# Kernel tuning notes

Measured on AMD Instinct MI355X. Metric: run time of the kernel, lower is better.

Reference implementation:

```python
import jax, jax.numpy as jnp
import numpy as np
from jax import lax

R = 0.7          # ball-query radius
K = 32           # max neighbors per ball
STRIDE = 32      # spatial stride -> M = N // STRIDE anchors
COUT = 1024      # mlp_planes[0]


def fps(pts, M):
    """Furthest point sampling. pts: [N,3] -> int32 [M] indices (starts at 0, like CUDA FPS)."""
    N = pts.shape[0]

    def step(carry, _):
        d2, last = carry
        dist = jnp.sum((pts - pts[last]) ** 2, axis=-1)
        d2 = jnp.minimum(d2, dist)
        return (d2, jnp.argmax(d2).astype(jnp.int32)), last

    init = (jnp.full((N,), 1e10, dtype=pts.dtype), jnp.int32(0))
    _, idxs = lax.scan(step, init, None, length=M)
    return idxs


def ball_query(neigh, anchor):
    """neigh: [N,3], anchor: [M,3] -> int32 [M,K]: first K in-radius neighbor indices,
    padded with the first valid index (matching pointnet2 ball_query semantics)."""
    N = neigh.shape[0]
    d2 = jnp.sum((anchor[:, None, :] - neigh[None, :, :]) ** 2, axis=-1)  # [M,N]
    key = jnp.where(d2 < R * R, jnp.arange(N), N)  # valid points keep their position
    order = jnp.argsort(key, axis=-1)[:, :K]       # stable: first-in-order valid indices
    valid = jnp.take_along_axis(key, order, axis=-1) < N
    return jnp.where(valid, order, order[:, :1])


def setup_inputs() -> dict:
    key = jax.random.key(0)
    k1, k2 = jax.random.split(key)
    xyzs = jax.random.uniform(k1, (4, 16, 2048, 3), dtype=jnp.float32)  # points in unit cube
    w_d = jax.random.normal(k2, (COUT, 4), dtype=jnp.float32) * 0.1     # conv_d 1x1 weight
    return {"xyzs": xyzs, "w_d": w_d}


def reference(xyzs, w_d):
    B, T, N, _ = xyzs.shape
    M = N // STRIDE
    # replicate temporal padding [1,1]
    pad = jnp.concatenate([xyzs[:, :1], xyzs, xyzs[:, -1:]], axis=1)  # [B,T+2,N,3]

    anchors_src = pad[:, 1:-1].reshape(B * T, N, 3)
    aidx = jax.vmap(lambda p: fps(p, M))(anchors_src)                         # [BT,M]
    anchor = jnp.take_along_axis(anchors_src, aidx[..., None], axis=1)        # [BT,M,3]

    feat = None
    for dt in (-1, 0, 1):  # temporal kernel taps
        neigh = pad[:, 1 + dt: 1 + dt + T].reshape(B * T, N, 3)
        idx = jax.vmap(ball_query)(neigh, anchor)                             # [BT,M,K]
        grouped = jnp.take_along_axis(
            neigh, idx.reshape(B * T, M * K)[..., None], axis=1
        ).reshape(B * T, M, K, 3)
        disp = grouped - anchor[:, :, None, :]                                # xyz displacement
        d4 = jnp.concatenate(
            [disp, jnp.full((B * T, M, K, 1), float(dt), disp.dtype)], axis=-1
        )                                                                     # [BT,M,K,4]
        f = jax.nn.relu(jnp.einsum('nmkc,oc->nmko', d4, w_d))                 # 1x1 conv + ReLU
        f = jnp.max(f, axis=2)                                                # spatial max pool -> [BT,M,C]
        feat = f if feat is None else feat + f                                # temporal sum pool

    new_xyzs = anchor.reshape(B, T, M, 3)
    new_features = feat.reshape(B, T, M, COUT).transpose(0, 1, 3, 2)          # [B,T,C,M]
    return new_xyzs, new_features
```

## Files before the change

kernel.cpp:

```cpp
#include <hip/hip_runtime.h>
#include <hip/hip_fp16.h>

#define NB 4
#define NT 16
#define NN 2048
#define NM 64
#define NK 32
#define NC 1024

static __device__ inline __half2 h2max(__half2 a, __half2 b) {
    unsigned int ai = *(unsigned int*)&a, bi = *(unsigned int*)&b, di;
    asm("v_pk_max_f16 %0, %1, %2" : "=v"(di) : "v"(ai), "v"(bi));
    return *(__half2*)&di;
}
static __device__ inline unsigned long long u64max(unsigned long long a, unsigned long long b) {
    return a > b ? a : b;
}

#define DPP_MAX_STEP(v, ctrl)                                                   \
    do {                                                                        \
        const int _mv = __builtin_amdgcn_update_dpp(                            \
            __float_as_int(v), __float_as_int(v), (ctrl), 0xf, 0xf, false);     \
        (v) = fmaxf((v), __int_as_float(_mv));                                  \
    } while (0)

__global__ __launch_bounds__(256) void fps_kernel(const float* __restrict__ xyzs,
                                                  float* __restrict__ out_xyz) {
    const int bt = blockIdx.x;
    const float* pts = xyzs + (size_t)bt * NN * 3;
    __shared__ __align__(16) float sP[NN * 3];
    __shared__ unsigned long long sPart[2][4];
    __shared__ float sAnchor[NM * 3];
    const int tid = threadIdx.x;
    const int lane = tid & 63, wave = tid >> 6;
    float wpt[24];
    {
        const float4* pv = (const float4*)pts + (size_t)tid * 6;
        #pragma unroll
        for (int i = 0; i < 6; ++i) {
            const float4 f = pv[i];
            ((float4*)sP)[tid * 6 + i] = f;
            wpt[4 * i + 0] = f.x; wpt[4 * i + 1] = f.y; wpt[4 * i + 2] = f.z; wpt[4 * i + 3] = f.w;
        }
    }
    float px[8], py[8], pz[8], d2[8];
    #pragma unroll
    for (int j = 0; j < 8; ++j) {
        px[j] = wpt[3 * j + 0]; py[j] = wpt[3 * j + 1]; pz[j] = wpt[3 * j + 2];
        d2[j] = 1e10f;
    }
    __syncthreads();
    int last = 0;
    for (int it = 0; it < NM; ++it) {
        const float lx = sP[last * 3 + 0], ly = sP[last * 3 + 1], lz = sP[last * 3 + 2];
        if (tid == 0) {
            sAnchor[it * 3 + 0] = lx; sAnchor[it * 3 + 1] = ly; sAnchor[it * 3 + 2] = lz;
        }
        float bv = -1.0f; int bp = 0;
        #pragma unroll
        for (int j = 0; j < 8; ++j) {
            const float dx = __fsub_rn(px[j], lx), dy = __fsub_rn(py[j], ly), dz = __fsub_rn(pz[j], lz);
            const float d = __fadd_rn(__fadd_rn(__fmul_rn(dx, dx), __fmul_rn(dy, dy)), __fmul_rn(dz, dz));
            d2[j] = fminf(d2[j], d);
            if (d2[j] > bv) { bv = d2[j]; bp = tid * 8 + j; }
        }
        float v = bv;
        DPP_MAX_STEP(v, 0x111);
        DPP_MAX_STEP(v, 0x112);
        DPP_MAX_STEP(v, 0x114);
        DPP_MAX_STEP(v, 0x118);
        DPP_MAX_STEP(v, 0x142);
        DPP_MAX_STEP(v, 0x143);
        const float vmax = __int_as_float(__builtin_amdgcn_readlane(__float_as_int(v), 63));
        const unsigned long long tied = __ballot(bv == vmax);
        const int srcLane = (int)(__ffsll((long long)tied) - 1);
        const int idxw = __shfl(bp, srcLane, 64);
        if (lane == 0)
            sPart[it & 1][wave] = ((unsigned long long)__float_as_uint(vmax) << 32)
                                | (unsigned)(NN - 1 - idxw);
        __syncthreads();
        const unsigned long long key =
            u64max(u64max(sPart[it & 1][0], sPart[it & 1][1]),
                   u64max(sPart[it & 1][2], sPart[it & 1][3]));
        last = NN - 1 - (int)(key & 0xffffffffull);
    }
    __syncthreads();
    for (int i = tid; i < NM * 3; i += 256)
        out_xyz[bt * NM * 3 + i] = sAnchor[i];
}

__global__ __launch_bounds__(256) void bq_kernel(const float* __restrict__ xyzs,
                                                 const float* __restrict__ anchors,
                                                 unsigned int* __restrict__ disp) {
    const int tid = threadIdx.x;
    const int lane = tid & 63, w = tid >> 6;
    const int q = blockIdx.x * 4 + w;
    const int bt = q / (NM * 3);
    const int r = q - bt * (NM * 3);
    const int m = r / 3, tap = r - m * 3;
    const int b = bt >> 4, t = bt & 15;
    __shared__ float sD[4][3][NK];
    const float ax = anchors[(bt * NM + m) * 3 + 0];
    const float ay = anchors[(bt * NM + m) * 3 + 1];
    const float az = anchors[(bt * NM + m) * 3 + 2];
    int tsrc = t + tap - 1;
    tsrc = tsrc < 0 ? 0 : (tsrc > NT - 1 ? NT - 1 : tsrc);
    const float* npts = xyzs + ((size_t)(b * NT + tsrc)) * NN * 3;
    int cnt = 0;
    for (int rr = 0; rr < NN / 64 && cnt < NK; ++rr) {
        const int n = rr * 64 + lane;
        const float dx = __fsub_rn(npts[n * 3 + 0], ax);
        const float dy = __fsub_rn(npts[n * 3 + 1], ay);
        const float dz = __fsub_rn(npts[n * 3 + 2], az);
        const float d2v = __fadd_rn(__fadd_rn(__fmul_rn(dx, dx), __fmul_rn(dy, dy)), __fmul_rn(dz, dz));
        const bool valid = d2v < 0.49f;
        const unsigned long long mask = __ballot(valid);
        const int pos = cnt + (int)__popcll(mask & ((1ull << lane) - 1ull));
        if (valid && pos < NK) {
            sD[w][0][pos] = dx; sD[w][1][pos] = dy; sD[w][2][pos] = dz;
        }
        cnt += (int)__popcll(mask);
    }
    if (cnt < NK) {
        float fx, fy, fz;
        if (cnt > 0) {
            fx = sD[w][0][0]; fy = sD[w][1][0]; fz = sD[w][2][0];
        } else {
            fx = __fsub_rn(npts[0], ax); fy = __fsub_rn(npts[1], ay); fz = __fsub_rn(npts[2], az);
        }
        if (lane >= cnt && lane < NK) {
            sD[w][0][lane] = fx; sD[w][1][lane] = fy; sD[w][2][lane] = fz;
        }
    }
    if (lane < 48) {
        const int c = lane >> 4, j = lane & 15;
        const __half2 hv = __float22half2_rn(make_float2(sD[w][c][2 * j], sD[w][c][2 * j + 1]));
        disp[(size_t)q * 48 + lane] = *(const unsigned int*)&hv;
    }
}

__global__ __launch_bounds__(256) void conv_kernel(const unsigned int* __restrict__ disp,
                                                   const float* __restrict__ wd,
                                                   float* __restrict__ feat) {
    const int blk = blockIdx.x;
    const int bt = blk >> 4;
    const int inner = blk & 15;
    const int mh = inner >> 2, cq = inner & 3;
    const int tid = threadIdx.x;
    const int lane = tid & 63, w = tid >> 6;
    const int m0 = mh * 16 + w * 4;
    const int c0 = cq * 256 + lane;
    float4 wv[4]; __half2 wx[4], wy[4], wz[4];
    #pragma unroll
    for (int r = 0; r < 4; ++r) {
        wv[r] = ((const float4*)wd)[c0 + 64 * r];
        wx[r] = __float2half2_rn(wv[r].x);
        wy[r] = __float2half2_rn(wv[r].y);
        wz[r] = __float2half2_rn(wv[r].z);
    }
    float acc[4][4];
    #pragma unroll
    for (int r = 0; r < 4; ++r)
        #pragma unroll
        for (int mi = 0; mi < 4; ++mi) acc[r][mi] = 0.0f;

    #pragma unroll
    for (int mi = 0; mi < 4; ++mi) {
        #pragma unroll
        for (int tap = 0; tap < 3; ++tap) {
            const uint4* dp = (const uint4*)(disp + ((size_t)((bt * NM + m0 + mi) * 3 + tap)) * 48);
            uint4 u[12];
            #pragma unroll
            for (int i = 0; i < 12; ++i) u[i] = dp[i];
            const unsigned int* uw = (const unsigned int*)u;
            __half2 a[4];
            #pragma unroll
            for (int j = 0; j < 16; ++j) {
                const __half2 hx = *(const __half2*)&uw[j];
                const __half2 hy = *(const __half2*)&uw[16 + j];
                const __half2 hz = *(const __half2*)&uw[32 + j];
                #pragma unroll
                for (int r = 0; r < 4; ++r) {
                    const __half2 s = __hfma2(wx[r], hx, __hfma2(wy[r], hy, __hmul2(wz[r], hz)));
                    a[r] = (j == 0) ? s : h2max(a[r], s);
                }
            }
            const float dtf = (float)(tap - 1);
            #pragma unroll
            for (int r = 0; r < 4; ++r) {
                const float mx = fmaxf(__low2float(a[r]), __high2float(a[r]));
                acc[r][mi] += fmaxf(0.0f, mx + wv[r].w * dtf);
            }
        }
    }
    #pragma unroll
    for (int r = 0; r < 4; ++r) {
        float* dst = feat + ((size_t)bt * NC + c0 + 64 * r) * NM + m0;
        *(float4*)dst = make_float4(acc[r][0], acc[r][1], acc[r][2], acc[r][3]);
    }
}

extern "C" void kernel_launch(void* const* d_in, const int* in_sizes, int n_in,
                              void* d_out, int out_size, void* d_ws, size_t ws_size,
                              hipStream_t stream) {
    const float* xyzs = (const float*)d_in[0];
    const float* wd   = (const float*)d_in[1];
    float* out_xyz = (float*)d_out;
    float* featp   = out_xyz + NB * NT * NM * 3;
    unsigned int* dispw = (unsigned int*)d_ws;
    hipLaunchKernelGGL(fps_kernel, dim3(NB * NT), dim3(256), 0, stream, xyzs, out_xyz);
    hipLaunchKernelGGL(bq_kernel, dim3(NB * NT * NM * 3 / 4), dim3(256), 0, stream,
                       xyzs, out_xyz, dispw);
    hipLaunchKernelGGL(conv_kernel, dim3(1024), dim3(256), 0, stream,
                       dispw, wd, featp);
}
```

Measured before the change: 123.6 us.

## Carry FPS winner coordinates through reduction and halve conv per-block work

```diff
diff --git a/kernel.cpp b/kernel.cpp
--- a/kernel.cpp
+++ b/kernel.cpp
@@ -13,9 +13,6 @@
     asm("v_pk_max_f16 %0, %1, %2" : "=v"(di) : "v"(ai), "v"(bi));
     return *(__half2*)&di;
 }
-static __device__ inline unsigned long long u64max(unsigned long long a, unsigned long long b) {
-    return a > b ? a : b;
-}
 
 #define DPP_MAX_STEP(v, ctrl)                                                   \
     do {                                                                        \
@@ -24,13 +21,18 @@
         (v) = fmaxf((v), __int_as_float(_mv));                                  \
     } while (0)
 
+static __device__ inline float readlane_f(float x, int l) {
+    return __int_as_float(__builtin_amdgcn_readlane(__float_as_int(x), l));
+}
+
 __global__ __launch_bounds__(256) void fps_kernel(const float* __restrict__ xyzs,
                                                   float* __restrict__ out_xyz) {
     const int bt = blockIdx.x;
     const float* pts = xyzs + (size_t)bt * NN * 3;
-    __shared__ __align__(16) float sP[NN * 3];
-    __shared__ unsigned long long sPart[2][4];
+    __shared__ unsigned long long sKey[2][4];
+    __shared__ __align__(16) float sCand[2][4][4];
     __shared__ float sAnchor[NM * 3];
+    __shared__ float sInit[3];
     const int tid = threadIdx.x;
     const int lane = tid & 63, wave = tid >> 6;
     float wpt[24];
@@ -39,30 +41,29 @@
         #pragma unroll
         for (int i = 0; i < 6; ++i) {
             const float4 f = pv[i];
-            ((float4*)sP)[tid * 6 + i] = f;
             wpt[4 * i + 0] = f.x; wpt[4 * i + 1] = f.y; wpt[4 * i + 2] = f.z; wpt[4 * i + 3] = f.w;
         }
     }
-    float px[8], py[8], pz[8], d2[8];
+    float px[8], py[8], pz[8], d2v[8];
     #pragma unroll
     for (int j = 0; j < 8; ++j) {
         px[j] = wpt[3 * j + 0]; py[j] = wpt[3 * j + 1]; pz[j] = wpt[3 * j + 2];
-        d2[j] = 1e10f;
-    }
+        d2v[j] = 1e10f;
+    }
+    if (tid == 0) { sInit[0] = px[0]; sInit[1] = py[0]; sInit[2] = pz[0]; }
     __syncthreads();
-    int last = 0;
+    float ax = sInit[0], ay = sInit[1], az = sInit[2];
     for (int it = 0; it < NM; ++it) {
-        const float lx = sP[last * 3 + 0], ly = sP[last * 3 + 1], lz = sP[last * 3 + 2];
         if (tid == 0) {
-            sAnchor[it * 3 + 0] = lx; sAnchor[it * 3 + 1] = ly; sAnchor[it * 3 + 2] = lz;
-        }
-        float bv = -1.0f; int bp = 0;
+            sAnchor[it * 3 + 0] = ax; sAnchor[it * 3 + 1] = ay; sAnchor[it * 3 + 2] = az;
+        }
+        float bv = -1.0f; int bj = 0;
         #pragma unroll
         for (int j = 0; j < 8; ++j) {
-            const float dx = __fsub_rn(px[j], lx), dy = __fsub_rn(py[j], ly), dz = __fsub_rn(pz[j], lz);
+            const float dx = __fsub_rn(px[j], ax), dy = __fsub_rn(py[j], ay), dz = __fsub_rn(pz[j], az);
             const float d = __fadd_rn(__fadd_rn(__fmul_rn(dx, dx), __fmul_rn(dy, dy)), __fmul_rn(dz, dz));
-            d2[j] = fminf(d2[j], d);
-            if (d2[j] > bv) { bv = d2[j]; bp = tid * 8 + j; }
+            d2v[j] = fminf(d2v[j], d);
+            if (d2v[j] > bv) { bv = d2v[j]; bj = j; }
         }
         float v = bv;
         DPP_MAX_STEP(v, 0x111);
@@ -71,18 +72,42 @@
         DPP_MAX_STEP(v, 0x118);
         DPP_MAX_STEP(v, 0x142);
         DPP_MAX_STEP(v, 0x143);
-        const float vmax = __int_as_float(__builtin_amdgcn_readlane(__float_as_int(v), 63));
+        const float vmax = readlane_f(v, 63);
         const unsigned long long tied = __ballot(bv == vmax);
-        const int srcLane = (int)(__ffsll((long long)tied) - 1);
-        const int idxw = __shfl(bp, srcLane, 64);
-        if (lane == 0)
-            sPart[it & 1][wave] = ((unsigned long long)__float_as_uint(vmax) << 32)
-                                | (unsigned)(NN - 1 - idxw);
+        const int src = (int)(__ffsll((long long)tied) - 1);
+        const float cx0 = (bj & 1) ? px[1] : px[0], cx1 = (bj & 1) ? px[3] : px[2];
+        const float cx2 = (bj & 1) ? px[5] : px[4], cx3 = (bj & 1) ? px[7] : px[6];
+        const float cy0 = (bj & 1) ? py[1] : py[0], cy1 = (bj & 1) ? py[3] : py[2];
+        const float cy2 = (bj & 1) ? py[5] : py[4], cy3 = (bj & 1) ? py[7] : py[6];
+        const float cz0 = (bj & 1) ? pz[1] : pz[0], cz1 = (bj & 1) ? pz[3] : pz[2];
+        const float cz2 = (bj & 1) ? pz[5] : pz[4], cz3 = (bj & 1) ? pz[7] : pz[6];
+        const float cxa = (bj & 2) ? cx1 : cx0, cxb = (bj & 2) ? cx3 : cx2;
+        const float cya = (bj & 2) ? cy1 : cy0, cyb = (bj & 2) ? cy3 : cy2;
+        const float cza = (bj & 2) ? cz1 : cz0, czb = (bj & 2) ? cz3 : cz2;
+        const float cx = (bj & 4) ? cxb : cxa;
+        const float cy = (bj & 4) ? cyb : cya;
+        const float cz = (bj & 4) ? czb : cza;
+        const int idx = tid * 8 + bj;
+        const int widx = __builtin_amdgcn_readlane(idx, src);
+        const float wx = readlane_f(cx, src);
+        const float wy = readlane_f(cy, src);
+        const float wz = readlane_f(cz, src);
+        const int par = it & 1;
+        if (lane == 0) {
+            sKey[par][wave] = ((unsigned long long)__float_as_uint(vmax) << 32)
+                            | (unsigned)(NN - 1 - widx);
+            *(float4*)&sCand[par][wave][0] = make_float4(wx, wy, wz, 0.0f);
+        }
         __syncthreads();
-        const unsigned long long key =
-            u64max(u64max(sPart[it & 1][0], sPart[it & 1][1]),
-                   u64max(sPart[it & 1][2], sPart[it & 1][3]));
-        last = NN - 1 - (int)(key & 0xffffffffull);
+        unsigned long long bk = sKey[par][0];
+        float4 bc = *(const float4*)&sCand[par][0][0];
+        #pragma unroll
+        for (int i = 1; i < 4; ++i) {
+            const unsigned long long ki = sKey[par][i];
+            const float4 ci = *(const float4*)&sCand[par][i][0];
+            if (ki > bk) { bk = ki; bc = ci; }
+        }
+        ax = bc.x; ay = bc.y; az = bc.z;
     }
     __syncthreads();
     for (int i = tid; i < NM * 3; i += 256)
@@ -139,64 +164,68 @@
     }
 }
 
-__global__ __launch_bounds__(256) void conv_kernel(const unsigned int* __restrict__ disp,
-                                                   const float* __restrict__ wd,
-                                                   float* __restrict__ feat) {
+__global__ __launch_bounds__(256, 8) void conv_kernel(const unsigned int* __restrict__ disp,
+                                                      const float* __restrict__ wd,
+                                                      float* __restrict__ feat) {
     const int blk = blockIdx.x;
-    const int bt = blk >> 4;
-    const int inner = blk & 15;
+    const int bt = blk >> 5;
+    const int inner = blk & 31;
     const int mh = inner >> 2, cq = inner & 3;
     const int tid = threadIdx.x;
     const int lane = tid & 63, w = tid >> 6;
-    const int m0 = mh * 16 + w * 4;
+    const int m0 = mh * 8 + w * 2;
     const int c0 = cq * 256 + lane;
-    float4 wv[4]; __half2 wx[4], wy[4], wz[4];
+    __half2 wx[4], wy[4], wz[4]; float ww[4];
     #pragma unroll
     for (int r = 0; r < 4; ++r) {
-        wv[r] = ((const float4*)wd)[c0 + 64 * r];
-        wx[r] = __float2half2_rn(wv[r].x);
-        wy[r] = __float2half2_rn(wv[r].y);
-        wz[r] = __float2half2_rn(wv[r].z);
-    }
-    float acc[4][4];
-    #pragma unroll
-    for (int r = 0; r < 4; ++r)
-        #pragma unroll
-        for (int mi = 0; mi < 4; ++mi) acc[r][mi] = 0.0f;
-
-    #pragma unroll
-    for (int mi = 0; mi < 4; ++mi) {
+        const float4 wv = ((const float4*)wd)[c0 + 64 * r];
+        wx[r] = __float2half2_rn(wv.x);
+        wy[r] = __float2half2_rn(wv.y);
+        wz[r] = __float2half2_rn(wv.z);
+        ww[r] = wv.w;
+    }
+    float acc[4][2];
+    #pragma unroll
+    for (int r = 0; r < 4; ++r) { acc[r][0] = 0.0f; acc[r][1] = 0.0f; }
+
+    #pragma unroll
+    for (int mi = 0; mi < 2; ++mi) {
         #pragma unroll
         for (int tap = 0; tap < 3; ++tap) {
             const uint4* dp = (const uint4*)(disp + ((size_t)((bt * NM + m0 + mi) * 3 + tap)) * 48);
-            uint4 u[12];
-            #pragma unroll
-            for (int i = 0; i < 12; ++i) u[i] = dp[i];
-            const unsigned int* uw = (const unsigned int*)u;
             __half2 a[4];
             #pragma unroll
-            for (int j = 0; j < 16; ++j) {
-                const __half2 hx = *(const __half2*)&uw[j];
-                const __half2 hy = *(const __half2*)&uw[16 + j];
-                const __half2 hz = *(const __half2*)&uw[32 + j];
+            for (int h = 0; h < 2; ++h) {
+                const uint4 ux0 = dp[2 * h],     ux1 = dp[2 * h + 1];
+                const uint4 uy0 = dp[4 + 2 * h], uy1 = dp[5 + 2 * h];
+                const uint4 uz0 = dp[8 + 2 * h], uz1 = dp[9 + 2 * h];
+                const unsigned int X[8] = {ux0.x, ux0.y, ux0.z, ux0.w, ux1.x, ux1.y, ux1.z, ux1.w};
+                const unsigned int Y[8] = {uy0.x, uy0.y, uy0.z, uy0.w, uy1.x, uy1.y, uy1.z, uy1.w};
+                const unsigned int Z[8] = {uz0.x, uz0.y, uz0.z, uz0.w, uz1.x, uz1.y, uz1.z, uz1.w};
                 #pragma unroll
-                for (int r = 0; r < 4; ++r) {
-                    const __half2 s = __hfma2(wx[r], hx, __hfma2(wy[r], hy, __hmul2(wz[r], hz)));
-                    a[r] = (j == 0) ? s : h2max(a[r], s);
+                for (int j = 0; j < 8; ++j) {
+                    const __half2 hx = *(const __half2*)&X[j];
+                    const __half2 hy = *(const __half2*)&Y[j];
+                    const __half2 hz = *(const __half2*)&Z[j];
+                    #pragma unroll
+                    for (int r = 0; r < 4; ++r) {
+                        const __half2 s = __hfma2(wx[r], hx, __hfma2(wy[r], hy, __hmul2(wz[r], hz)));
+                        a[r] = (h == 0 && j == 0) ? s : h2max(a[r], s);
+                    }
                 }
             }
             const float dtf = (float)(tap - 1);
             #pragma unroll
             for (int r = 0; r < 4; ++r) {
                 const float mx = fmaxf(__low2float(a[r]), __high2float(a[r]));
-                acc[r][mi] += fmaxf(0.0f, mx + wv[r].w * dtf);
+                acc[r][mi] += fmaxf(0.0f, mx + ww[r] * dtf);
             }
         }
     }
     #pragma unroll
     for (int r = 0; r < 4; ++r) {
         float* dst = feat + ((size_t)bt * NC + c0 + 64 * r) * NM + m0;
-        *(float4*)dst = make_float4(acc[r][0], acc[r][1], acc[r][2], acc[r][3]);
+        *(float2*)dst = make_float2(acc[r][0], acc[r][1]);
     }
 }
 
@@ -211,6 +240,6 @@
     hipLaunchKernelGGL(fps_kernel, dim3(NB * NT), dim3(256), 0, stream, xyzs, out_xyz);
     hipLaunchKernelGGL(bq_kernel, dim3(NB * NT * NM * 3 / 4), dim3(256), 0, stream,
                        xyzs, out_xyz, dispw);
-    hipLaunchKernelGGL(conv_kernel, dim3(1024), dim3(256), 0, stream,
+    hipLaunchKernelGGL(conv_kernel, dim3(2048), dim3(256), 0, stream,
                        dispw, wd, featp);
 }
```

New measurement: 132.6 us. 7.3% more time.

## Run FPS in a single wavefront to drop per-iteration block barriers

Applied to the files above, without the earlier changes.

```diff
diff --git a/kernel.cpp b/kernel.cpp
--- a/kernel.cpp
+++ b/kernel.cpp
@@ -13,9 +13,6 @@
     asm("v_pk_max_f16 %0, %1, %2" : "=v"(di) : "v"(ai), "v"(bi));
     return *(__half2*)&di;
 }
-static __device__ inline unsigned long long u64max(unsigned long long a, unsigned long long b) {
-    return a > b ? a : b;
-}
 
 #define DPP_MAX_STEP(v, ctrl)                                                   \
     do {                                                                        \
@@ -24,46 +21,62 @@
         (v) = fmaxf((v), __int_as_float(_mv));                                  \
     } while (0)
 
-__global__ __launch_bounds__(256) void fps_kernel(const float* __restrict__ xyzs,
-                                                  float* __restrict__ out_xyz) {
+static __device__ inline float readlane_f(float x, int l) {
+    return __int_as_float(__builtin_amdgcn_readlane(__float_as_int(x), l));
+}
+
+__global__ __launch_bounds__(64, 1) void fps_kernel(const float* __restrict__ xyzs,
+                                                    float* __restrict__ out_xyz) {
     const int bt = blockIdx.x;
     const float* pts = xyzs + (size_t)bt * NN * 3;
     __shared__ __align__(16) float sP[NN * 3];
-    __shared__ unsigned long long sPart[2][4];
-    __shared__ float sAnchor[NM * 3];
-    const int tid = threadIdx.x;
-    const int lane = tid & 63, wave = tid >> 6;
-    float wpt[24];
+    const int lane = threadIdx.x;
+    float arr[96];
     {
-        const float4* pv = (const float4*)pts + (size_t)tid * 6;
-        #pragma unroll
-        for (int i = 0; i < 6; ++i) {
+        const float4* pv = (const float4*)pts + (size_t)lane * 24;
+        #pragma unroll
+        for (int i = 0; i < 24; ++i) {
             const float4 f = pv[i];
-            ((float4*)sP)[tid * 6 + i] = f;
-            wpt[4 * i + 0] = f.x; wpt[4 * i + 1] = f.y; wpt[4 * i + 2] = f.z; wpt[4 * i + 3] = f.w;
-        }
-    }
-    float px[8], py[8], pz[8], d2[8];
-    #pragma unroll
-    for (int j = 0; j < 8; ++j) {
-        px[j] = wpt[3 * j + 0]; py[j] = wpt[3 * j + 1]; pz[j] = wpt[3 * j + 2];
-        d2[j] = 1e10f;
-    }
-    __syncthreads();
-    int last = 0;
+            ((float4*)sP)[lane * 24 + i] = f;
+            arr[4 * i + 0] = f.x; arr[4 * i + 1] = f.y; arr[4 * i + 2] = f.z; arr[4 * i + 3] = f.w;
+        }
+    }
+    float px[32], py[32], pz[32], d2[32];
+    #pragma unroll
+    for (int p = 0; p < 32; ++p) {
+        px[p] = arr[3 * p + 0]; py[p] = arr[3 * p + 1]; pz[p] = arr[3 * p + 2];
+        d2[p] = 1e10f;
+    }
+    float ax = readlane_f(px[0], 0), ay = readlane_f(py[0], 0), az = readlane_f(pz[0], 0);
     for (int it = 0; it < NM; ++it) {
-        const float lx = sP[last * 3 + 0], ly = sP[last * 3 + 1], lz = sP[last * 3 + 2];
-        if (tid == 0) {
-            sAnchor[it * 3 + 0] = lx; sAnchor[it * 3 + 1] = ly; sAnchor[it * 3 + 2] = lz;
-        }
-        float bv = -1.0f; int bp = 0;
-        #pragma unroll
-        for (int j = 0; j < 8; ++j) {
-            const float dx = __fsub_rn(px[j], lx), dy = __fsub_rn(py[j], ly), dz = __fsub_rn(pz[j], lz);
+        if (lane < 3) {
+            const float val = lane == 0 ? ax : (lane == 1 ? ay : az);
+            out_xyz[(bt * NM + it) * 3 + lane] = val;
+        }
+        #pragma unroll
+        for (int p = 0; p < 32; ++p) {
+            const float dx = __fsub_rn(px[p], ax), dy = __fsub_rn(py[p], ay), dz = __fsub_rn(pz[p], az);
             const float d = __fadd_rn(__fadd_rn(__fmul_rn(dx, dx), __fmul_rn(dy, dy)), __fmul_rn(dz, dz));
-            d2[j] = fminf(d2[j], d);
-            if (d2[j] > bv) { bv = d2[j]; bp = tid * 8 + j; }
-        }
+            d2[p] = fminf(d2[p], d);
+        }
+        float t16[16], t8[8], t4[4], t2[2];
+        #pragma unroll
+        for (int i = 0; i < 16; ++i) t16[i] = fmaxf(d2[i], d2[i + 16]);
+        #pragma unroll
+        for (int i = 0; i < 8; ++i) t8[i] = fmaxf(t16[i], t16[i + 8]);
+        #pragma unroll
+        for (int i = 0; i < 4; ++i) t4[i] = fmaxf(t8[i], t8[i + 4]);
+        t2[0] = fmaxf(t4[0], t4[2]); t2[1] = fmaxf(t4[1], t4[3]);
+        const float bv = fmaxf(t2[0], t2[1]);
+        int bq0 = 64, bq1 = 64, bq2 = 64, bq3 = 64;
+        #pragma unroll
+        for (int jj = 7; jj >= 0; --jj) {
+            bq0 = (d2[jj] == bv) ? jj : bq0;
+            bq1 = (d2[8 + jj] == bv) ? (8 + jj) : bq1;
+            bq2 = (d2[16 + jj] == bv) ? (16 + jj) : bq2;
+            bq3 = (d2[24 + jj] == bv) ? (24 + jj) : bq3;
+        }
+        const int bj = min(min(bq0, bq1), min(bq2, bq3));
         float v = bv;
         DPP_MAX_STEP(v, 0x111);
         DPP_MAX_STEP(v, 0x112);
@@ -71,22 +84,12 @@
         DPP_MAX_STEP(v, 0x118);
         DPP_MAX_STEP(v, 0x142);
         DPP_MAX_STEP(v, 0x143);
-        const float vmax = __int_as_float(__builtin_amdgcn_readlane(__float_as_int(v), 63));
+        const float vmax = readlane_f(v, 63);
         const unsigned long long tied = __ballot(bv == vmax);
-        const int srcLane = (int)(__ffsll((long long)tied) - 1);
-        const int idxw = __shfl(bp, srcLane, 64);
-        if (lane == 0)
-            sPart[it & 1][wave] = ((unsigned long long)__float_as_uint(vmax) << 32)
-                                | (unsigned)(NN - 1 - idxw);
-        __syncthreads();
-        const unsigned long long key =
-            u64max(u64max(sPart[it & 1][0], sPart[it & 1][1]),
-                   u64max(sPart[it & 1][2], sPart[it & 1][3]));
-        last = NN - 1 - (int)(key & 0xffffffffull);
-    }
-    __syncthreads();
-    for (int i = tid; i < NM * 3; i += 256)
-        out_xyz[bt * NM * 3 + i] = sAnchor[i];
+        const int src = (int)(__ffsll((long long)tied) - 1);
+        const int last = __builtin_amdgcn_readlane(lane * 32 + bj, src);
+        ax = sP[3 * last + 0]; ay = sP[3 * last + 1]; az = sP[3 * last + 2];
+    }
 }
 
 __global__ __launch_bounds__(256) void bq_kernel(const float* __restrict__ xyzs,
@@ -208,7 +211,7 @@
     float* out_xyz = (float*)d_out;
     float* featp   = out_xyz + NB * NT * NM * 3;
     unsigned int* dispw = (unsigned int*)d_ws;
-    hipLaunchKernelGGL(fps_kernel, dim3(NB * NT), dim3(256), 0, stream, xyzs, out_xyz);
+    hipLaunchKernelGGL(fps_kernel, dim3(NB * NT), dim3(64), 0, stream, xyzs, out_xyz);
     hipLaunchKernelGGL(bq_kernel, dim3(NB * NT * NM * 3 / 4), dim3(256), 0, stream,
                        xyzs, out_xyz, dispw);
     hipLaunchKernelGGL(conv_kernel, dim3(1024), dim3(256), 0, stream,
```

New measurement: 148.0 us. 19.8% more time.
